# Performance work log

Measured on AMD Instinct MI355X. Metric: run time of the kernel, lower is better.

## Reference

```python
import jax, jax.numpy as jnp
import numpy as np

N = 20000      # nodes
E = 640000     # edges (avg degree 32)
F = 6          # feature_dim
D = 128        # weight_dim
L = 3          # lstm num_layers
DEPTH = 10     # extra iterations after initial call


def setup_inputs() -> dict:
    key = jax.random.key(0)
    ks = jax.random.split(key, 10)
    s = 0.05
    return {
        "features": jax.random.normal(ks[0], (N, F), jnp.float32),
        "src": jax.random.randint(ks[1], (E,), 0, N),
        "dst": jax.random.randint(ks[2], (E,), 0, N),
        "W_in": jax.random.normal(ks[3], (F, D), jnp.float32) * s,
        "b_in": jnp.zeros((D,), jnp.float32),
        "Wih0": jax.random.normal(ks[4], (4 * D, 2 * D), jnp.float32) * s,   # layer 0: input = concat(h_in, feat)
        "Wih_rest": jax.random.normal(ks[5], (2, 4 * D, D), jnp.float32) * s,  # layers 1,2
        "Whh": jax.random.normal(ks[6], (L, 4 * D, D), jnp.float32) * s,
        "bih": jnp.zeros((L, 4 * D), jnp.float32),
        "bhh": jnp.zeros((L, 4 * D), jnp.float32),
        "W_out": jax.random.normal(ks[7], (D, 1), jnp.float32) * s,
        "b_out": jnp.zeros((1,), jnp.float32),
    }


def _lstm_cell(x, h, c, Wih, Whh, b):
    # PyTorch gate order: i, f, g, o
    gates = x @ Wih.T + h @ Whh.T + b              # [N, 4D]
    i, f, g, o = jnp.split(gates, 4, axis=-1)
    i = jax.nn.sigmoid(i)
    f = jax.nn.sigmoid(f)
    o = jax.nn.sigmoid(o)
    g = jnp.tanh(g)
    c_new = f * c + i * g
    h_new = o * jnp.tanh(c_new)
    return h_new, c_new


def reference(features, src, dst, W_in, b_in, Wih0, Wih_rest, Whh, bih, bhh, W_out, b_out):
    n = features.shape[0]
    b = bih + bhh                                   # [L, 4D]

    def agg(x):
        # DGL update_all(copy_src, mean): mean over incoming edges (src -> dst)
        s = jax.ops.segment_sum(x[src], dst, num_segments=n)
        deg = jax.ops.segment_sum(jnp.ones((src.shape[0],), x.dtype), dst, num_segments=n)
        return jnp.where(deg[:, None] > 0, s / jnp.maximum(deg, 1.0)[:, None], 0.0)

    feat = jax.nn.relu(features @ W_in + b_in)      # [N, D]
    h = jnp.zeros((L, n, D), features.dtype)
    c = jnp.zeros((L, n, D), features.dtype)

    def step(carry, _):
        feat, h, c = carry
        x0 = jnp.concatenate([agg(feat), feat], axis=-1)   # [N, 2D]
        h0, c0 = _lstm_cell(x0, h[0], c[0], Wih0, Whh[0], b[0])
        h1, c1 = _lstm_cell(h0, h[1], c[1], Wih_rest[0], Whh[1], b[1])
        h2, c2 = _lstm_cell(h1, h[2], c[2], Wih_rest[1], Whh[2], b[2])
        return (h2, jnp.stack([h0, h1, h2]), jnp.stack([c0, c1, c2])), None

    # initial call + depth extra iterations, all structurally identical
    (feat, h, c), _ = jax.lax.scan(step, (feat, h, c), None, length=1 + DEPTH)
    return h[-1] @ W_out + b_out                    # [N, 1]
```

## Files before the change

kernel.cpp:

```cpp
#include <hip/hip_runtime.h>
#include <math.h>

typedef _Float16 f16;
typedef __attribute__((ext_vector_type(8))) _Float16 half8;
typedef __attribute__((ext_vector_type(4))) float float4v;

__device__ __forceinline__ float fast_sigmoid(float x) { return 1.0f / (1.0f + __expf(-x)); }
__device__ __forceinline__ float fast_tanh(float x) {
    float a = fabsf(x);
    float e = __expf(-2.0f * a);
    float t = (1.0f - e) / (1.0f + e);
    return copysignf(t, x);
}

__device__ __forceinline__ void async_copy16(const void* gsrc, void* ldst) {
    __builtin_amdgcn_global_load_lds(
        (const __attribute__((address_space(1))) void*)gsrc,
        (__attribute__((address_space(3))) void*)ldst,
        16, 0, 0);
}

__global__ void packb_kernel(const float* __restrict__ Wih, int Kih,
                             const float* __restrict__ Whh, int K,
                             const float* __restrict__ bih, const float* __restrict__ bhh,
                             f16* __restrict__ Bp, float* __restrict__ bp) {
    int t = blockIdx.x * blockDim.x + threadIdx.x;
    if (t >= (K << 9)) return;
    int colp = t / K;
    int k = t - colp * K;
    int dg = colp >> 6, q = (colp >> 4) & 3, dl = colp & 15;
    int j = q * 128 + dg * 16 + dl;
    float v = (k < Kih) ? Wih[j * Kih + k] : Whh[j * (K - Kih) + (k - Kih)];
    Bp[t] = (f16)v;
    if (k == 0) bp[colp] = bih[j] + bhh[j];
}

__global__ void feat0_kernel(const float* __restrict__ features, const float* __restrict__ W_in,
                             const float* __restrict__ b_in, f16* __restrict__ feat, int n) {
    int t = blockIdx.x * blockDim.x + threadIdx.x;
    if (t >= n * 128) return;
    int node = t >> 7;
    int d = t & 127;
    float s = b_in[d];
#pragma unroll
    for (int k = 0; k < 6; ++k) s += features[node * 6 + k] * W_in[k * 128 + d];
    feat[t] = (f16)fmaxf(s, 0.0f);
}

__global__ void hist_kernel(const int* __restrict__ dst, int* __restrict__ cnt, int e) {
    int t = blockIdx.x * blockDim.x + threadIdx.x;
    if (t < e) atomicAdd(&cnt[dst[t]], 1);
}

__global__ void scan_kernel(const int* __restrict__ cnt, int* __restrict__ off,
                            int* __restrict__ cur, float* __restrict__ recip, int n) {
    __shared__ int sums[1024];
    int t = threadIdx.x;
    int chunk = (n + 1023) >> 10;
    int s0 = t * chunk;
    int s1 = s0 + chunk; if (s1 > n) s1 = n;
    int s = 0;
    for (int i = s0; i < s1; ++i) s += cnt[i];
    sums[t] = s;
    __syncthreads();
    if (t == 0) {
        int acc = 0;
        for (int i = 0; i < 1024; ++i) { int v = sums[i]; sums[i] = acc; acc += v; }
        off[n] = acc;
    }
    __syncthreads();
    int acc = sums[t];
    for (int i = s0; i < s1; ++i) {
        off[i] = acc; cur[i] = acc;
        int c = cnt[i];
        recip[i] = (c > 0) ? 1.0f / (float)c : 0.0f;
        acc += c;
    }
}

__global__ void scatter_kernel(const int* __restrict__ src, const int* __restrict__ dst,
                               int* __restrict__ cur, int* __restrict__ esrc, int e) {
    int t = blockIdx.x * blockDim.x + threadIdx.x;
    if (t >= e) return;
    int d = dst[t];
    int p = atomicAdd(&cur[d], 1);
    esrc[p] = src[t];
}

__global__ void agg_kernel(const f16* __restrict__ feat, const int* __restrict__ off,
                           const int* __restrict__ esrc, const float* __restrict__ recip,
                           f16* __restrict__ agg, int n) {
    int slot = threadIdx.x >> 4;
    int lane = threadIdx.x & 15;
    int v = blockIdx.x * 16 + slot;
    if (v >= n) return;
    int e0 = off[v], e1 = off[v + 1];
    float a[8];
#pragma unroll
    for (int j = 0; j < 8; ++j) a[j] = 0.0f;
    int e = e0;
    for (; e + 4 <= e1; e += 4) {
        int s0 = esrc[e], s1 = esrc[e + 1], s2 = esrc[e + 2], s3 = esrc[e + 3];
        half8 v0 = *(const half8*)&feat[(size_t)s0 * 128 + lane * 8];
        half8 v1 = *(const half8*)&feat[(size_t)s1 * 128 + lane * 8];
        half8 v2 = *(const half8*)&feat[(size_t)s2 * 128 + lane * 8];
        half8 v3 = *(const half8*)&feat[(size_t)s3 * 128 + lane * 8];
#pragma unroll
        for (int j = 0; j < 8; ++j)
            a[j] += (float)v0[j] + (float)v1[j] + (float)v2[j] + (float)v3[j];
    }
    for (; e < e1; ++e) {
        int s = esrc[e];
        half8 v0 = *(const half8*)&feat[(size_t)s * 128 + lane * 8];
#pragma unroll
        for (int j = 0; j < 8; ++j) a[j] += (float)v0[j];
    }
    float r = recip[v];
    half8 o;
#pragma unroll
    for (int j = 0; j < 8; ++j) o[j] = (f16)(a[j] * r);
    *(half8*)&agg[(size_t)v * 128 + lane * 8] = o;
}

#define BM 64

template <int PARTS>
__global__ __launch_bounds__(256, 3) void gemm_lstm(
    const f16* __restrict__ A0, const f16* __restrict__ A1, const f16* __restrict__ A2,
    const f16* __restrict__ Bp, const float* __restrict__ bp,
    const float* __restrict__ c_in, float* __restrict__ c_out, f16* __restrict__ h_out,
    int nrows) {
    constexpr int K = PARTS * 128;
    __shared__ f16 As[64 * 32];
    __shared__ f16 Bs[256 * 32];

    const int tid = threadIdx.x;
    const int w = tid >> 6;
    const int lane = tid & 63;
    const int dl = lane & 15;
    const int quad = lane >> 4;
    const int row0 = blockIdx.x * BM;
    const int cb = blockIdx.y;

    float4v acc[4][4];
#pragma unroll
    for (int q = 0; q < 4; ++q) {
        float b = bp[cb * 256 + w * 64 + q * 16 + dl];
#pragma unroll
        for (int rt = 0; rt < 4; ++rt) {
            acc[rt][q][0] = b; acc[rt][q][1] = b; acc[rt][q][2] = b; acc[rt][q][3] = b;
        }
    }

    const int srow = lane >> 2;
    const int soff = (lane & 3) * 8;

    for (int kt = 0; kt < PARTS * 4; ++kt) {
        const f16* Ap = A0;
        const int pi = kt >> 2;
        if (PARTS >= 2 && pi == 1) Ap = A1;
        if (PARTS >= 3 && pi == 2) Ap = A2;
        const int kk = (kt & 3) * 32;

        __syncthreads();
        async_copy16(&Ap[(size_t)(row0 + w * 16 + srow) * 128 + kk + soff],
                     (f16*)As + w * 512);
        const f16* Bbase = Bp + (size_t)(cb * 256) * K + kt * 32;
#pragma unroll
        for (int i = 0; i < 4; ++i) {
            int m = i * 4 + w;
            async_copy16(&Bbase[(size_t)(m * 16 + srow) * K + soff], (f16*)Bs + m * 512);
        }
        __syncthreads();

        half8 a[4], b[4];
#pragma unroll
        for (int rt = 0; rt < 4; ++rt)
            a[rt] = *(const half8*)&As[(rt * 16 + dl) * 32 + quad * 8];
#pragma unroll
        for (int q = 0; q < 4; ++q)
            b[q] = *(const half8*)&Bs[((w * 4 + q) * 16 + dl) * 32 + quad * 8];
#pragma unroll
        for (int rt = 0; rt < 4; ++rt)
#pragma unroll
            for (int q = 0; q < 4; ++q)
                acc[rt][q] = __builtin_amdgcn_mfma_f32_16x16x32_f16(a[rt], b[q], acc[rt][q], 0, 0, 0);
    }

    const int d = cb * 64 + w * 16 + dl;
#pragma unroll
    for (int rt = 0; rt < 4; ++rt) {
#pragma unroll
        for (int r = 0; r < 4; ++r) {
            int n = row0 + rt * 16 + quad * 4 + r;
            if (n < nrows) {
                float ig = fast_sigmoid(acc[rt][0][r]);
                float fg = fast_sigmoid(acc[rt][1][r]);
                float gg = fast_tanh(acc[rt][2][r]);
                float og = fast_sigmoid(acc[rt][3][r]);
                float cold = c_in[(size_t)n * 128 + d];
                float cn = fg * cold + ig * gg;
                c_out[(size_t)n * 128 + d] = cn;
                h_out[(size_t)n * 128 + d] = (f16)(og * fast_tanh(cn));
            }
        }
    }
}

__global__ void out_kernel(const f16* __restrict__ h2, const float* __restrict__ Wout,
                           const float* __restrict__ bout, float* __restrict__ out) {
    int n = blockIdx.x;
    int l = threadIdx.x;
    float v = (float)h2[(size_t)n * 128 + l] * Wout[l] +
              (float)h2[(size_t)n * 128 + 64 + l] * Wout[64 + l];
#pragma unroll
    for (int o = 32; o > 0; o >>= 1) v += __shfl_down(v, o, 64);
    if (l == 0) out[n] = v + bout[0];
}

extern "C" void kernel_launch(void* const* d_in, const int* in_sizes, int n_in,
                              void* d_out, int out_size, void* d_ws, size_t ws_size,
                              hipStream_t stream) {
    const float* features = (const float*)d_in[0];
    const int*   src      = (const int*)d_in[1];
    const int*   dst      = (const int*)d_in[2];
    const float* W_in     = (const float*)d_in[3];
    const float* b_in     = (const float*)d_in[4];
    const float* Wih0     = (const float*)d_in[5];
    const float* Wih_rest = (const float*)d_in[6];
    const float* Whh      = (const float*)d_in[7];
    const float* bih      = (const float*)d_in[8];
    const float* bhh      = (const float*)d_in[9];
    const float* W_out    = (const float*)d_in[10];
    const float* b_out    = (const float*)d_in[11];
    float* out = (float*)d_out;

    const int N = in_sizes[0] / 6;
    const int E = in_sizes[1];
    const int NP = N + BM;

    char* ws = (char*)d_ws;
    size_t pos = 0;
    auto alloc = [&](size_t bytes) -> void* {
        void* p = ws + pos;
        pos = (pos + bytes + 255) & ~(size_t)255;
        return p;
    };
    const size_t hrow = 128;
    const size_t hbytes = (size_t)NP * hrow * sizeof(f16);
    const size_t cbytes = (size_t)NP * hrow * sizeof(float);
    f16* feath = (f16*)alloc(hbytes);
    f16* aggh  = (f16*)alloc(hbytes);
    f16* hblk  = (f16*)alloc(3 * hbytes);
    f16* h0 = hblk + 0 * (size_t)NP * hrow;
    f16* h1 = hblk + 1 * (size_t)NP * hrow;
    f16* h2 = hblk + 2 * (size_t)NP * hrow;
    float* cblk = (float*)alloc(3 * cbytes);
    float* c0 = cblk + 0 * (size_t)NP * hrow;
    float* c1 = cblk + 1 * (size_t)NP * hrow;
    float* c2 = cblk + 2 * (size_t)NP * hrow;
    f16* Bp0 = (f16*)alloc((size_t)512 * 384 * sizeof(f16));
    f16* Bp1 = (f16*)alloc((size_t)512 * 256 * sizeof(f16));
    f16* Bp2 = (f16*)alloc((size_t)512 * 256 * sizeof(f16));
    float* bp0 = (float*)alloc(512 * sizeof(float));
    float* bp1 = (float*)alloc(512 * sizeof(float));
    float* bp2 = (float*)alloc(512 * sizeof(float));
    int*   cnt   = (int*)alloc((size_t)N * 4);
    int*   offs  = (int*)alloc((size_t)(N + 1) * 4);
    int*   cur   = (int*)alloc((size_t)N * 4);
    int*   esrc  = (int*)alloc((size_t)E * 4);
    float* recip = (float*)alloc((size_t)N * 4);

    hipMemsetAsync(hblk, 0, 3 * hbytes, stream);
    hipMemsetAsync(cblk, 0, 3 * cbytes, stream);
    hipMemsetAsync(cnt, 0, (size_t)N * 4, stream);

    packb_kernel<<<(512 * 384 + 255) / 256, 256, 0, stream>>>(
        Wih0, 256, Whh, 384, bih, bhh, Bp0, bp0);
    packb_kernel<<<(512 * 256 + 255) / 256, 256, 0, stream>>>(
        Wih_rest, 128, Whh + 512 * 128, 256, bih + 512, bhh + 512, Bp1, bp1);
    packb_kernel<<<(512 * 256 + 255) / 256, 256, 0, stream>>>(
        Wih_rest + 512 * 128, 128, Whh + 2 * 512 * 128, 256, bih + 1024, bhh + 1024, Bp2, bp2);

    feat0_kernel<<<(N * 128 + 255) / 256, 256, 0, stream>>>(features, W_in, b_in, feath, N);
    hist_kernel<<<(E + 255) / 256, 256, 0, stream>>>(dst, cnt, E);
    scan_kernel<<<1, 1024, 0, stream>>>(cnt, offs, cur, recip, N);
    scatter_kernel<<<(E + 255) / 256, 256, 0, stream>>>(src, dst, cur, esrc, E);

    const dim3 ggrid((N + BM - 1) / BM, 2, 1);
    const int gagg = (N + 15) / 16;
    const f16* featcur = feath;
    for (int step = 0; step < 11; ++step) {
        agg_kernel<<<gagg, 256, 0, stream>>>(featcur, offs, esrc, recip, aggh, N);
        gemm_lstm<3><<<ggrid, 256, 0, stream>>>(aggh, featcur, h0, Bp0, bp0, c0, c0, h0, N);
        gemm_lstm<2><<<ggrid, 256, 0, stream>>>(h0, h1, nullptr, Bp1, bp1, c1, c1, h1, N);
        gemm_lstm<2><<<ggrid, 256, 0, stream>>>(h1, h2, nullptr, Bp2, bp2, c2, c2, h2, N);
        featcur = h2;
    }
    out_kernel<<<N, 64, 0, stream>>>(h2, W_out, b_out, out);
}
```

Baseline: 1.127 ms.

## Fuse three LSTM layer GEMMs into one per-step kernel with swizzled LDS

Replaces the three per-layer gemm_lstm launches with one fused_lstm_step kernel. Each 64-row block now computes all 512 gate columns and runs the three layers back to back, which is valid because each layer only reads the rows it owns. The A operand is loaded straight from global memory into registers, and B tiles go to LDS with an XOR swizzle to cut bank conflicts. This removes two launches per step and the duplicated A reads across column blocks, at the cost of half as many blocks (313 on 256 CUs, so poor wave balance), more accumulator registers per thread and lower occupancy. The one-time scan kernel also switches to a wavefront-shuffle prefix sum.

```diff
diff --git a/kernel.cpp b/kernel.cpp
--- a/kernel.cpp
+++ b/kernel.cpp
@@ -54,28 +54,37 @@
 
 __global__ void scan_kernel(const int* __restrict__ cnt, int* __restrict__ off,
                             int* __restrict__ cur, float* __restrict__ recip, int n) {
-    __shared__ int sums[1024];
+    __shared__ int wsum[16];
     int t = threadIdx.x;
     int chunk = (n + 1023) >> 10;
     int s0 = t * chunk;
     int s1 = s0 + chunk; if (s1 > n) s1 = n;
+    if (s0 > n) s0 = n;
     int s = 0;
     for (int i = s0; i < s1; ++i) s += cnt[i];
-    sums[t] = s;
+    int lane = t & 63, wv = t >> 6;
+    int v = s;
+#pragma unroll
+    for (int o = 1; o < 64; o <<= 1) {
+        int u = __shfl_up(v, o, 64);
+        if (lane >= o) v += u;
+    }
+    if (lane == 63) wsum[wv] = v;
     __syncthreads();
     if (t == 0) {
-        int acc = 0;
-        for (int i = 0; i < 1024; ++i) { int v = sums[i]; sums[i] = acc; acc += v; }
-        off[n] = acc;
+        int a = 0;
+#pragma unroll
+        for (int i = 0; i < 16; ++i) { int x = wsum[i]; wsum[i] = a; a += x; }
     }
     __syncthreads();
-    int acc = sums[t];
+    int acc = wsum[wv] + v - s;
     for (int i = s0; i < s1; ++i) {
         off[i] = acc; cur[i] = acc;
-        int c = cnt[i];
-        recip[i] = (c > 0) ? 1.0f / (float)c : 0.0f;
-        acc += c;
-    }
+        int cc = cnt[i];
+        recip[i] = cc > 0 ? 1.0f / (float)cc : 0.0f;
+        acc += cc;
+    }
+    if (t == 1023) off[n] = acc;
 }
 
 __global__ void scatter_kernel(const int* __restrict__ src, const int* __restrict__ dst,
@@ -124,87 +133,106 @@
 
 #define BM 64
 
-template <int PARTS>
-__global__ __launch_bounds__(256, 3) void gemm_lstm(
-    const f16* __restrict__ A0, const f16* __restrict__ A1, const f16* __restrict__ A2,
+template <int KT>
+__device__ __forceinline__ void layer_run(
+    const f16* A0, const f16* A1, const f16* A2,
     const f16* __restrict__ Bp, const float* __restrict__ bp,
-    const float* __restrict__ c_in, float* __restrict__ c_out, f16* __restrict__ h_out,
-    int nrows) {
-    constexpr int K = PARTS * 128;
-    __shared__ f16 As[64 * 32];
-    __shared__ f16 Bs[256 * 32];
-
+    float* c, f16* h,
+    f16* Bs, int row0, int nrows) {
+    constexpr int K = KT * 32;
     const int tid = threadIdx.x;
     const int w = tid >> 6;
     const int lane = tid & 63;
     const int dl = lane & 15;
     const int quad = lane >> 4;
-    const int row0 = blockIdx.x * BM;
-    const int cb = blockIdx.y;
-
-    float4v acc[4][4];
-#pragma unroll
-    for (int q = 0; q < 4; ++q) {
-        float b = bp[cb * 256 + w * 64 + q * 16 + dl];
+
+    float4v acc[4][8];
+#pragma unroll
+    for (int j = 0; j < 8; ++j) {
+        float b = bp[w * 128 + j * 16 + dl];
 #pragma unroll
         for (int rt = 0; rt < 4; ++rt) {
-            acc[rt][q][0] = b; acc[rt][q][1] = b; acc[rt][q][2] = b; acc[rt][q][3] = b;
+            acc[rt][j][0] = b; acc[rt][j][1] = b; acc[rt][j][2] = b; acc[rt][j][3] = b;
         }
     }
 
-    const int srow = lane >> 2;
-    const int soff = (lane & 3) * 8;
-
-    for (int kt = 0; kt < PARTS * 4; ++kt) {
+    const int sdl = lane >> 2;
+    const int sj = lane & 3;
+    const int sg = sj ^ (sdl & 3);
+    const int rdoff = (dl << 5) + ((quad ^ (dl & 3)) << 3);
+
+    for (int kt = 0; kt < KT; ++kt) {
         const f16* Ap = A0;
         const int pi = kt >> 2;
-        if (PARTS >= 2 && pi == 1) Ap = A1;
-        if (PARTS >= 3 && pi == 2) Ap = A2;
+        if (pi == 1) Ap = A1;
+        if (pi == 2) Ap = A2;
         const int kk = (kt & 3) * 32;
 
         __syncthreads();
-        async_copy16(&Ap[(size_t)(row0 + w * 16 + srow) * 128 + kk + soff],
-                     (f16*)As + w * 512);
-        const f16* Bbase = Bp + (size_t)(cb * 256) * K + kt * 32;
-#pragma unroll
-        for (int i = 0; i < 4; ++i) {
-            int m = i * 4 + w;
-            async_copy16(&Bbase[(size_t)(m * 16 + srow) * K + soff], (f16*)Bs + m * 512);
+#pragma unroll
+        for (int i = 0; i < 8; ++i) {
+            int m = (w << 3) + i;
+            async_copy16(Bp + (size_t)(m * 16 + sdl) * K + kt * 32 + (sg << 3),
+                         Bs + (m << 9));
         }
+        half8 a[4];
+#pragma unroll
+        for (int rt = 0; rt < 4; ++rt)
+            a[rt] = *(const half8*)&Ap[(size_t)(row0 + rt * 16 + dl) * 128 + kk + (quad << 3)];
         __syncthreads();
 
-        half8 a[4], b[4];
-#pragma unroll
-        for (int rt = 0; rt < 4; ++rt)
-            a[rt] = *(const half8*)&As[(rt * 16 + dl) * 32 + quad * 8];
-#pragma unroll
-        for (int q = 0; q < 4; ++q)
-            b[q] = *(const half8*)&Bs[((w * 4 + q) * 16 + dl) * 32 + quad * 8];
-#pragma unroll
-        for (int rt = 0; rt < 4; ++rt)
-#pragma unroll
-            for (int q = 0; q < 4; ++q)
-                acc[rt][q] = __builtin_amdgcn_mfma_f32_16x16x32_f16(a[rt], b[q], acc[rt][q], 0, 0, 0);
-    }
-
-    const int d = cb * 64 + w * 16 + dl;
-#pragma unroll
-    for (int rt = 0; rt < 4; ++rt) {
-#pragma unroll
-        for (int r = 0; r < 4; ++r) {
-            int n = row0 + rt * 16 + quad * 4 + r;
-            if (n < nrows) {
-                float ig = fast_sigmoid(acc[rt][0][r]);
-                float fg = fast_sigmoid(acc[rt][1][r]);
-                float gg = fast_tanh(acc[rt][2][r]);
-                float og = fast_sigmoid(acc[rt][3][r]);
-                float cold = c_in[(size_t)n * 128 + d];
-                float cn = fg * cold + ig * gg;
-                c_out[(size_t)n * 128 + d] = cn;
-                h_out[(size_t)n * 128 + d] = (f16)(og * fast_tanh(cn));
+#pragma unroll
+        for (int hh = 0; hh < 2; ++hh) {
+            half8 b[4];
+#pragma unroll
+            for (int q = 0; q < 4; ++q) {
+                int m = (w << 3) + (hh << 2) + q;
+                b[q] = *(const half8*)&Bs[(m << 9) + rdoff];
+            }
+#pragma unroll
+            for (int rt = 0; rt < 4; ++rt)
+#pragma unroll
+                for (int q = 0; q < 4; ++q)
+                    acc[rt][(hh << 2) + q] =
+                        __builtin_amdgcn_mfma_f32_16x16x32_f16(a[rt], b[q], acc[rt][(hh << 2) + q], 0, 0, 0);
+        }
+    }
+
+#pragma unroll
+    for (int hh = 0; hh < 2; ++hh) {
+        const int d = ((w << 1) + hh) * 16 + dl;
+#pragma unroll
+        for (int rt = 0; rt < 4; ++rt) {
+#pragma unroll
+            for (int r = 0; r < 4; ++r) {
+                int n = row0 + rt * 16 + (quad << 2) + r;
+                if (n < nrows) {
+                    float ig = fast_sigmoid(acc[rt][(hh << 2) + 0][r]);
+                    float fg = fast_sigmoid(acc[rt][(hh << 2) + 1][r]);
+                    float gg = fast_tanh(acc[rt][(hh << 2) + 2][r]);
+                    float og = fast_sigmoid(acc[rt][(hh << 2) + 3][r]);
+                    float cold = c[(size_t)n * 128 + d];
+                    float cn = fg * cold + ig * gg;
+                    c[(size_t)n * 128 + d] = cn;
+                    h[(size_t)n * 128 + d] = (f16)(og * fast_tanh(cn));
+                }
             }
         }
     }
+}
+
+__global__ __launch_bounds__(256, 2) void fused_lstm_step(
+    const f16* __restrict__ aggb, const f16* __restrict__ feat,
+    f16* h0, f16* h1, f16* h2,
+    float* c0, float* c1, float* c2,
+    const f16* __restrict__ B0, const f16* __restrict__ B1, const f16* __restrict__ B2,
+    const float* __restrict__ bp0, const float* __restrict__ bp1, const float* __restrict__ bp2,
+    int nrows) {
+    __shared__ f16 Bs[512 * 32];
+    const int row0 = blockIdx.x * BM;
+    layer_run<12>(aggb, feat, h0, B0, bp0, c0, h0, Bs, row0, nrows);
+    layer_run<8>(h0, h1, nullptr, B1, bp1, c1, h1, Bs, row0, nrows);
+    layer_run<8>(h1, h2, nullptr, B2, bp2, c2, h2, Bs, row0, nrows);
 }
 
 __global__ void out_kernel(const f16* __restrict__ h2, const float* __restrict__ Wout,
@@ -287,14 +315,13 @@
     scan_kernel<<<1, 1024, 0, stream>>>(cnt, offs, cur, recip, N);
     scatter_kernel<<<(E + 255) / 256, 256, 0, stream>>>(src, dst, cur, esrc, E);
 
-    const dim3 ggrid((N + BM - 1) / BM, 2, 1);
+    const int gx = (N + BM - 1) / BM;
     const int gagg = (N + 15) / 16;
     const f16* featcur = feath;
     for (int step = 0; step < 11; ++step) {
         agg_kernel<<<gagg, 256, 0, stream>>>(featcur, offs, esrc, recip, aggh, N);
-        gemm_lstm<3><<<ggrid, 256, 0, stream>>>(aggh, featcur, h0, Bp0, bp0, c0, c0, h0, N);
-        gemm_lstm<2><<<ggrid, 256, 0, stream>>>(h0, h1, nullptr, Bp1, bp1, c1, c1, h1, N);
-        gemm_lstm<2><<<ggrid, 256, 0, stream>>>(h1, h2, nullptr, Bp2, bp2, c2, c2, h2, N);
+        fused_lstm_step<<<gx, 256, 0, stream>>>(aggh, featcur, h0, h1, h2, c0, c1, c2,
+                                                Bp0, Bp1, Bp2, bp0, bp1, bp2, N);
         featcur = h2;
     }
     out_kernel<<<N, 64, 0, stream>>>(h2, W_out, b_out, out);
```

New measurement: 1.514 ms. 34.3% more time.
